# Performance work log

Hardware: AMD Instinct MI355X
Metric: run time of the kernel (lower is better)

The kernel has to match this reference:

```python
import jax, jax.numpy as jnp
import numpy as np

B, S, HID, NH = 64, 197, 768, 12
DH = HID // NH  # 64
EPS = 1e-24


def setup_inputs() -> dict:
    key = jax.random.key(0)
    ks = jax.random.split(key, 20)
    def lin(i):
        w = jax.random.normal(ks[i], (HID, HID), jnp.float32) * 0.02  # stored [in, out]
        b = jnp.zeros((HID,), jnp.float32)
        return w, b
    Wmq, bmq = lin(0); Wcq, bcq = lin(1)
    Wmk, bmk = lin(2); Wck, bck = lin(3)
    Wmv, bmv = lin(4); Wcv, bcv = lin(5)
    Wmd, bmd = lin(6); Wcd, bcd = lin(7)
    return dict(
        input_mean_tensor=jax.random.normal(ks[8], (B, S, HID), jnp.float32),
        input_cov_tensor=jax.random.normal(ks[9], (B, S, HID), jnp.float32),
        Wmq=Wmq, bmq=bmq, Wcq=Wcq, bcq=bcq,
        Wmk=Wmk, bmk=bmk, Wck=Wck, bck=bck,
        Wmv=Wmv, bmv=bmv, Wcv=Wcv, bcv=bcv,
        Wmd=Wmd, bmd=bmd, Wcd=Wcd, bcd=bcd,
    )


def _heads(x):
    # [B, S, HID] -> [B, NH, S, DH]
    return x.reshape(x.shape[0], x.shape[1], NH, DH).transpose(0, 2, 1, 3)


def _merge(x):
    # [B, NH, S, DH] -> [B, S, HID]
    return x.transpose(0, 2, 1, 3).reshape(x.shape[0], x.shape[2], HID)


def wasserstein_distance_matmul(m1, c1, m2, c2):
    # all [B, NH, S, DH]; returns [B, NH, S, S]
    m1_2 = jnp.sum(m1 * m1, -1, keepdims=True)            # [B,NH,S,1]
    m2_2 = jnp.sum(m2 * m2, -1, keepdims=True)
    ret = m1_2 + jnp.swapaxes(m2_2, -1, -2) - 2.0 * jnp.einsum('bhqd,bhkd->bhqk', m1, m2)
    c1_2 = jnp.sum(c1, -1, keepdims=True)
    c2_2 = jnp.sum(c2, -1, keepdims=True)
    s1 = jnp.sqrt(jnp.clip(c1, EPS, None))
    s2 = jnp.sqrt(jnp.clip(c2, EPS, None))
    cov_ret = c1_2 + jnp.swapaxes(c2_2, -1, -2) - 2.0 * jnp.einsum('bhqd,bhkd->bhqk', s1, s2)
    return ret + cov_ret


def reference(input_mean_tensor, input_cov_tensor,
              Wmq, bmq, Wcq, bcq, Wmk, bmk, Wck, bck,
              Wmv, bmv, Wcv, bcv, Wmd, bmd, Wcd, bcd):
    mean_q = _heads(input_mean_tensor @ Wmq + bmq)
    mean_k = _heads(input_mean_tensor @ Wmk + bmk)
    mean_v = _heads(input_mean_tensor @ Wmv + bmv)
    cov_q = _heads(jax.nn.elu(input_cov_tensor @ Wcq + bcq) + 1.0)
    cov_k = _heads(jax.nn.elu(input_cov_tensor @ Wck + bck) + 1.0)
    cov_v = _heads(jax.nn.elu(input_cov_tensor @ Wcv + bcv) + 1.0)

    scores = -wasserstein_distance_matmul(mean_q, cov_q, mean_k, cov_k)
    scores = scores / jnp.sqrt(jnp.float32(DH))
    probs = jax.nn.softmax(scores, axis=-1)  # [B,NH,S,S]

    mean_ctx = _merge(jnp.einsum('bhqk,bhkd->bhqd', probs, mean_v))
    cov_ctx = _merge(jnp.einsum('bhqk,bhkd->bhqd', probs * probs, cov_v))

    mean_hidden = mean_ctx @ Wmd + bmd
    cov_hidden = cov_ctx @ Wcd + bcd
    return (mean_hidden, cov_hidden)
```

## Files before the change

### kernel.cpp

```cpp
#include <hip/hip_runtime.h>
#include <hip/hip_bf16.h>
#include <stdint.h>

typedef _Float16 f16;
typedef _Float16 f16x8 __attribute__((ext_vector_type(8)));
typedef _Float16 f16x4 __attribute__((ext_vector_type(4)));
typedef float f32x4 __attribute__((ext_vector_type(4)));

constexpr int B = 64, S = 197, HID = 768, NH = 12, DH = 64;
constexpr int M = B * S;
constexpr int Mpad = 12800;
constexpr int BNS = B * NH * S;
constexpr int VSTRIDE = 224;
constexpr size_t NPH = (size_t)Mpad * HID;
constexpr size_t MH = (size_t)M * HID;
constexpr size_t WSZ1 = (size_t)HID * HID;
constexpr size_t VTSZ = (size_t)B * NH * DH * VSTRIDE;

__device__ __forceinline__ f32x4 mfma16(f16x8 a, f16x8 b, f32x4 c) {
  return __builtin_amdgcn_mfma_f32_16x16x32_f16(a, b, c, 0, 0, 0);
}

__device__ __forceinline__ void gload16(const void* g, void* l) {
  __builtin_amdgcn_global_load_lds(
      (const __attribute__((address_space(1))) void*)g,
      (__attribute__((address_space(3))) void*)l, 16, 0, 0);
}

__device__ __forceinline__ int xcd_swizzle(int wg, int nwg) {
  const int q = nwg >> 3, r = nwg & 7;
  const int x = wg & 7, p = wg >> 3;
  return (x < r ? x * (q + 1) : r * (q + 1) + (x - r) * q) + p;
}

__global__ __launch_bounds__(256) void zero_kernel(char* __restrict__ p, size_t n16) {
  const size_t i = (size_t)blockIdx.x * 256 + threadIdx.x;
  if (i < n16) reinterpret_cast<int4*>(p)[i] = int4{0, 0, 0, 0};
}

__global__ __launch_bounds__(256) void cvt_x_kernel(
    const float* __restrict__ xm, const float* __restrict__ xc,
    f16* __restrict__ ym, f16* __restrict__ yc) {
  const size_t i8 = ((size_t)blockIdx.x * 256 + threadIdx.x) * 8;
  f16x8 vm = {}, vc = {};
  if (i8 < MH) {
    const float4 a0 = *reinterpret_cast<const float4*>(xm + i8);
    const float4 a1 = *reinterpret_cast<const float4*>(xm + i8 + 4);
    const float4 b0 = *reinterpret_cast<const float4*>(xc + i8);
    const float4 b1 = *reinterpret_cast<const float4*>(xc + i8 + 4);
    vm[0] = (f16)a0.x; vm[1] = (f16)a0.y; vm[2] = (f16)a0.z; vm[3] = (f16)a0.w;
    vm[4] = (f16)a1.x; vm[5] = (f16)a1.y; vm[6] = (f16)a1.z; vm[7] = (f16)a1.w;
    vc[0] = (f16)b0.x; vc[1] = (f16)b0.y; vc[2] = (f16)b0.z; vc[3] = (f16)b0.w;
    vc[4] = (f16)b1.x; vc[5] = (f16)b1.y; vc[6] = (f16)b1.z; vc[7] = (f16)b1.w;
  }
  *reinterpret_cast<f16x8*>(ym + i8) = vm;
  *reinterpret_cast<f16x8*>(yc + i8) = vc;
}

struct WPtrs { const float* w[8]; };

__global__ __launch_bounds__(256) void cvt_w_kernel(WPtrs p, f16* __restrict__ wt) {
  __shared__ float tile[32][33];
  const int z = blockIdx.z;
  const float* W = p.w[z];
  f16* Wt = wt + (size_t)z * WSZ1;
  const int k0 = blockIdx.x * 32, n0 = blockIdx.y * 32;
  const int tx = threadIdx.x & 31, ty = threadIdx.x >> 5;
#pragma unroll
  for (int i = 0; i < 4; ++i)
    tile[ty + i * 8][tx] = W[(size_t)(k0 + ty + i * 8) * HID + n0 + tx];
  __syncthreads();
#pragma unroll
  for (int i = 0; i < 4; ++i)
    Wt[(size_t)(n0 + ty + i * 8) * HID + k0 + tx] = (f16)tile[tx][ty + i * 8];
}

__device__ __forceinline__ void gemm_core(
    const f16* __restrict__ Abase, const f16* __restrict__ Btbase,
    int m0, int n0, int tid, char* lds, f32x4 (&acc)[8][4]) {
  const int w = tid >> 6, lane = tid & 63;
  const int l15 = lane & 15, lg = lane >> 4;
  const int wr = (w >> 2) * 128, wc = (w & 3) * 64;

  const int srow = w * 32 + (lane >> 2);
  const int scol = (lane & 3) * 16;
  const char* gA = reinterpret_cast<const char*>(Abase + (size_t)(m0 + srow) * HID) + scol;
  const char* gB = reinterpret_cast<const char*>(Btbase + (size_t)(n0 + srow) * HID) + scol;
  const int wbase = w * 2048;

#define STAGE_TILE(T, BUF)                                               \
  do {                                                                   \
    const size_t off_ = (size_t)(T) * 64;                                \
    char* la_ = lds + (BUF) * 32768 + wbase;                             \
    char* lb_ = la_ + 16384;                                             \
    gload16(gA + off_, la_);                                             \
    gload16(gA + off_ + (size_t)16 * 1536, la_ + 1024);                  \
    gload16(gB + off_, lb_);                                             \
    gload16(gB + off_ + (size_t)16 * 1536, lb_ + 1024);                  \
  } while (0)

  STAGE_TILE(0, 0);
  STAGE_TILE(1, 1);
  asm volatile("s_waitcnt vmcnt(4)\n\ts_barrier" ::: "memory");

#pragma unroll
  for (int t = 0; t < 24; ++t) {
    if (t + 2 < 24) STAGE_TILE(t + 2, (t + 2) % 3);

    const char* cA = lds + (t % 3) * 32768;
    const char* cB = cA + 16384;
    f16x8 af[8], bf[4];
#pragma unroll
    for (int fi = 0; fi < 8; ++fi)
      af[fi] = *reinterpret_cast<const f16x8*>(cA + (wr + l15 + fi * 16) * 64 + lg * 16);
#pragma unroll
    for (int fj = 0; fj < 4; ++fj)
      bf[fj] = *reinterpret_cast<const f16x8*>(cB + (wc + l15 + fj * 16) * 64 + lg * 16);

    __builtin_amdgcn_s_setprio(1);
#pragma unroll
    for (int fi = 0; fi < 8; ++fi)
#pragma unroll
      for (int fj = 0; fj < 4; ++fj)
        acc[fi][fj] = mfma16(af[fi], bf[fj], acc[fi][fj]);
    __builtin_amdgcn_s_setprio(0);

    if (t + 2 < 24) {
      asm volatile("s_waitcnt vmcnt(4)\n\ts_barrier" ::: "memory");
    } else if (t + 1 < 24) {
      asm volatile("s_waitcnt vmcnt(0)\n\ts_barrier" ::: "memory");
    }
  }
#undef STAGE_TILE
}

struct ProjArgs {
  const f16* A[2]; const f16* Bt[2];
  const float* bias[2][3];
  f16* out0[2];
  f16* out1[2];
  f16* vt[2];
  float* qterm; float* kterm;
};

__global__ __launch_bounds__(512, 1) void gemm_proj(ProjArgs g) {
  __shared__ alignas(16) char lds[98304];
  const int swz = xcd_swizzle(blockIdx.x, 900);
  const int z = swz / 450;
  const int rest = swz - z * 450;
  const int x = rest / 9, y = rest - x * 9;
  const int m0 = x * 256, n0 = y * 256;

  f32x4 acc[8][4] = {};
  gemm_core(g.A[z], g.Bt[z], m0, n0, threadIdx.x, lds, acc);

  const int tid = threadIdx.x, w = tid >> 6, lane = tid & 63;
  const int l15 = lane & 15, lg = lane >> 4;
  const int wr = (w >> 2) * 128, wc = (w & 3) * 64;
  const int nsel = n0 / 768;
  const int colbase = (n0 - nsel * 768) + wc;
  const int rbase = m0 + wr + lg * 4;
  const float* bias = g.bias[z][nsel];
  const int hh = colbase >> 6;

  if (nsel < 2) {
    f16* Y = nsel ? g.out1[z] : g.out0[z];
    float* term = nsel ? g.kterm : g.qterm;
    float bv4[4];
#pragma unroll
    for (int fj = 0; fj < 4; ++fj) bv4[fj] = bias[colbase + l15 + fj * 16];
#pragma unroll
    for (int fi = 0; fi < 8; ++fi) {
#pragma unroll
      for (int r = 0; r < 4; ++r) {
        const int row = rbase + fi * 16 + r;
        float ssum = 0.f;
#pragma unroll
        for (int fj = 0; fj < 4; ++fj) {
          float v = acc[fi][fj][r] + bv4[fj];
          if (z == 1) { v = (v > 0.f) ? v + 1.f : __expf(v); v = sqrtf(v); }
          const f16 st = (f16)(v * 0.5f);
          if (row < M) Y[(size_t)row * HID + colbase + l15 + fj * 16] = st;
          const float sf = (float)st;
          ssum = fmaf(sf, sf, ssum);
        }
        ssum += __shfl_xor(ssum, 1, 64);
        ssum += __shfl_xor(ssum, 2, 64);
        ssum += __shfl_xor(ssum, 4, 64);
        ssum += __shfl_xor(ssum, 8, 64);
        if (l15 == 0 && row < M) {
          const int bb = row / S, ss = row - bb * S;
          atomicAdd(&term[(bb * NH + hh) * S + ss], 0.5f * ssum);
        }
      }
    }
  } else {
    f16* VT = g.vt[z];
#pragma unroll
    for (int fj = 0; fj < 4; ++fj) {
      const int col = colbase + l15 + fj * 16;
      const float bv = bias[col];
      const int dd = col & 63;
#pragma unroll
      for (int fi = 0; fi < 8; ++fi)
#pragma unroll
        for (int r = 0; r < 4; ++r) {
          const int row = rbase + fi * 16 + r;
          if (row < M) {
            float v = acc[fi][fj][r] + bv;
            if (z == 1) v = (v > 0.f) ? v + 1.f : __expf(v);
            const int bb = row / S, ss = row - bb * S;
            VT[((size_t)(bb * NH + hh) * DH + dd) * VSTRIDE + ss] = (f16)v;
          }
        }
    }
  }
}

struct OutArgs {
  const f16* A[2]; const f16* Bt[2]; const float* bias[2]; float* Y[2];
};

__global__ __launch_bounds__(512, 1) void gemm_out(OutArgs g) {
  __shared__ alignas(16) char lds[98304];
  const int swz = xcd_swizzle(blockIdx.x, 300);
  const int z = swz / 150;
  const int rest = swz - z * 150;
  const int x = rest / 3, y = rest - x * 3;
  const int m0 = x * 256, n0 = y * 256;

  f32x4 acc[8][4] = {};
  gemm_core(g.A[z], g.Bt[z], m0, n0, threadIdx.x, lds, acc);

  const int tid = threadIdx.x, w = tid >> 6, lane = tid & 63;
  const int l15 = lane & 15, lg = lane >> 4;
  const int wr = (w >> 2) * 128, wc = (w & 3) * 64;
  const int rbase = m0 + wr + lg * 4;
  float* Y = g.Y[z];
#pragma unroll
  for (int fj = 0; fj < 4; ++fj) {
    const int col = n0 + wc + l15 + fj * 16;
    const float bv = g.bias[z][col];
#pragma unroll
    for (int fi = 0; fi < 8; ++fi)
#pragma unroll
      for (int r = 0; r < 4; ++r) {
        const int row = rbase + fi * 16 + r;
        if (row < M) Y[(size_t)row * HID + col] = acc[fi][fj][r] + bv;
      }
  }
}

__global__ __launch_bounds__(256, 2) void attn_kernel(
    const f16* __restrict__ mq, const f16* __restrict__ sq,
    const f16* __restrict__ mk, const f16* __restrict__ sk,
    const f16* __restrict__ vtm, const f16* __restrict__ vtc,
    const float* __restrict__ qterm, const float* __restrict__ kterm,
    f16* __restrict__ mean_ctx, f16* __restrict__ cov_ctx) {
  __shared__ char Pb[64 * 512];
  __shared__ float qt_s[64];
  __shared__ float kt_s[256];
  __shared__ float red_m[4][64];
  __shared__ float red_s[4][64];

  const int swz = xcd_swizzle(blockIdx.x, 3072);
  const int qtile = swz & 3, bh = swz >> 2;
  const int h = bh % NH, b = bh / NH;
  const int s0 = qtile * 64;
  const int tid = threadIdx.x, w = tid >> 6, lane = tid & 63;
  const int l15 = lane & 15, lg = lane >> 4;

  const size_t base = (size_t)(b * S) * HID + (size_t)h * DH;
  const int tb = bh * S;

  f16x8 qmf[4][2], qsf[4][2];
#pragma unroll
  for (int fi = 0; fi < 4; ++fi) {
    const size_t o = base + (size_t)(s0 + fi * 16 + l15) * HID + lg * 8;
    qmf[fi][0] = *reinterpret_cast<const f16x8*>(mq + o);
    qmf[fi][1] = *reinterpret_cast<const f16x8*>(mq + o + 32);
    qsf[fi][0] = *reinterpret_cast<const f16x8*>(sq + o);
    qsf[fi][1] = *reinterpret_cast<const f16x8*>(sq + o + 32);
  }
  if (tid < 64) qt_s[tid] = (s0 + tid < S) ? qterm[tb + s0 + tid] : 0.f;
  kt_s[tid] = (tid < S) ? kterm[tb + tid] : 0.f;
  __syncthreads();

  f32x4 acc[4][4] = {};
  __builtin_amdgcn_s_setprio(1);
#pragma unroll
  for (int fj = 0; fj < 4; ++fj) {
    const size_t o = base + (size_t)(w * 64 + fj * 16 + l15) * HID + lg * 8;
    const f16x8 a0 = *reinterpret_cast<const f16x8*>(mk + o);
    const f16x8 a1 = *reinterpret_cast<const f16x8*>(mk + o + 32);
    const f16x8 c0 = *reinterpret_cast<const f16x8*>(sk + o);
    const f16x8 c1 = *reinterpret_cast<const f16x8*>(sk + o + 32);
#pragma unroll
    for (int fi = 0; fi < 4; ++fi) {
      acc[fj][fi] = mfma16(a0, qmf[fi][0], acc[fj][fi]);
      acc[fj][fi] = mfma16(c0, qsf[fi][0], acc[fj][fi]);
      acc[fj][fi] = mfma16(a1, qmf[fi][1], acc[fj][fi]);
      acc[fj][fi] = mfma16(c1, qsf[fi][1], acc[fj][fi]);
    }
  }
  __builtin_amdgcn_s_setprio(0);

  const int d = w * 16 + l15;
  const size_t vbase = ((size_t)bh * DH + d) * VSTRIDE + lg * 8;
  f16x8 vmr[7], vcr[7];
#pragma unroll
  for (int ks = 0; ks < 7; ++ks) {
    vmr[ks] = *reinterpret_cast<const f16x8*>(vtm + vbase + ks * 32);
    vcr[ks] = *reinterpret_cast<const f16x8*>(vtc + vbase + ks * 32);
  }

#pragma unroll
  for (int fi = 0; fi < 4; ++fi) {
    const float qv = qt_s[fi * 16 + l15];
    float mx = -1e30f;
#pragma unroll
    for (int fj = 0; fj < 4; ++fj)
#pragma unroll
      for (int r = 0; r < 4; ++r) {
        const int j = w * 64 + fj * 16 + lg * 4 + r;
        float sv = acc[fj][fi][r] - qv - kt_s[j];
        if (j >= S) sv = -1e30f;
        acc[fj][fi][r] = sv;
        mx = fmaxf(mx, sv);
      }
    mx = fmaxf(mx, __shfl_xor(mx, 16, 64));
    mx = fmaxf(mx, __shfl_xor(mx, 32, 64));
    if (lg == 0) red_m[w][fi * 16 + l15] = mx;
  }
  __syncthreads();

#pragma unroll
  for (int fi = 0; fi < 4; ++fi) {
    const int q = fi * 16 + l15;
    const float m = fmaxf(fmaxf(red_m[0][q], red_m[1][q]),
                          fmaxf(red_m[2][q], red_m[3][q]));
    const int xr = (q & 7) << 4;
    float sum = 0.f;
#pragma unroll
    for (int fj = 0; fj < 4; ++fj) {
      f16x4 p4;
#pragma unroll
      for (int r = 0; r < 4; ++r) {
        const float e = __expf(acc[fj][fi][r] - m);
        sum += e;
        p4[r] = (f16)e;
      }
      *reinterpret_cast<f16x4*>(
          Pb + q * 512 + ((2 * (w * 64 + fj * 16 + lg * 4)) ^ xr)) = p4;
    }
    sum += __shfl_xor(sum, 16, 64);
    sum += __shfl_xor(sum, 32, 64);
    if (lg == 0) red_s[w][q] = sum;
  }
  __syncthreads();

  f32x4 macc[4] = {}, cacc[4] = {};
  __builtin_amdgcn_s_setprio(1);
#pragma unroll
  for (int ks = 0; ks < 7; ++ks) {
#pragma unroll
    for (int fi = 0; fi < 4; ++fi) {
      const int q = fi * 16 + l15;
      const f16x8 pa = *reinterpret_cast<const f16x8*>(
          Pb + q * 512 + ((2 * (ks * 32 + lg * 8)) ^ ((q & 7) << 4)));
      macc[fi] = mfma16(pa, vmr[ks], macc[fi]);
      const f16x8 pq = pa * pa;
      cacc[fi] = mfma16(pq, vcr[ks], cacc[fi]);
    }
  }
  __builtin_amdgcn_s_setprio(0);

#pragma unroll
  for (int fi = 0; fi < 4; ++fi)
#pragma unroll
    for (int r = 0; r < 4; ++r) {
      const int qo = fi * 16 + lg * 4 + r;
      const int srow = s0 + qo;
      if (srow < S) {
        const float tot = red_s[0][qo] + red_s[1][qo] + red_s[2][qo] + red_s[3][qo];
        const float inv = 1.f / tot;
        const size_t oidx = (size_t)(b * S + srow) * HID + h * DH + d;
        mean_ctx[oidx] = (f16)(macc[fi][r] * inv);
        cov_ctx[oidx] = (f16)(cacc[fi][r] * inv * inv);
      }
    }
}

extern "C" void kernel_launch(void* const* d_in, const int* in_sizes, int n_in,
                              void* d_out, int out_size, void* d_ws, size_t ws_size,
                              hipStream_t stream) {
  const float* in_mean = (const float*)d_in[0];
  const float* in_cov = (const float*)d_in[1];
  const float* Wmq = (const float*)d_in[2];  const float* bmq = (const float*)d_in[3];
  const float* Wcq = (const float*)d_in[4];  const float* bcq = (const float*)d_in[5];
  const float* Wmk = (const float*)d_in[6];  const float* bmk = (const float*)d_in[7];
  const float* Wck = (const float*)d_in[8];  const float* bck = (const float*)d_in[9];
  const float* Wmv = (const float*)d_in[10]; const float* bmv = (const float*)d_in[11];
  const float* Wcv = (const float*)d_in[12]; const float* bcv = (const float*)d_in[13];
  const float* Wmd = (const float*)d_in[14]; const float* bmd = (const float*)d_in[15];
  const float* Wcd = (const float*)d_in[16]; const float* bcd = (const float*)d_in[17];

  const size_t need = (2 * NPH + 8 * WSZ1 + 4 * MH + 2 * VTSZ) * sizeof(f16) +
                      2 * (size_t)BNS * sizeof(float);
  if (ws_size < need) return;

  f16* Xm = (f16*)d_ws;
  f16* Xc = Xm + NPH;
  f16* Wt = Xc + NPH;
  f16* mq = Wt + 8 * WSZ1;
  f16* mk = mq + MH;
  f16* sq = mk + MH;
  f16* sk = sq + MH;
  f16* vtm = sk + MH;
  f16* vtc = vtm + VTSZ;
  float* qterm = (float*)(vtc + VTSZ);
  float* kterm = qterm + BNS;
  f16* mean_ctx = Xm;
  f16* cov_ctx = Xc;

  float* out_mean = (float*)d_out;
  float* out_cov = out_mean + MH;

  dim3 blk(256);

  const size_t zbytes = 2 * VTSZ * sizeof(f16) + 2 * (size_t)BNS * sizeof(float);
  const size_t n16 = zbytes / 16;
  zero_kernel<<<(int)((n16 + 255) / 256), blk, 0, stream>>>((char*)vtm, n16);

  cvt_x_kernel<<<(int)(NPH / 2048), blk, 0, stream>>>(in_mean, in_cov, Xm, Xc);

  WPtrs wp;
  wp.w[0] = Wmq; wp.w[1] = Wmk; wp.w[2] = Wmv;
  wp.w[3] = Wcq; wp.w[4] = Wck; wp.w[5] = Wcv;
  wp.w[6] = Wmd; wp.w[7] = Wcd;
  cvt_w_kernel<<<dim3(24, 24, 8), blk, 0, stream>>>(wp, Wt);

  ProjArgs pa;
  pa.A[0] = Xm; pa.A[1] = Xc;
  pa.Bt[0] = Wt; pa.Bt[1] = Wt + 3 * WSZ1;
  pa.bias[0][0] = bmq; pa.bias[0][1] = bmk; pa.bias[0][2] = bmv;
  pa.bias[1][0] = bcq; pa.bias[1][1] = bck; pa.bias[1][2] = bcv;
  pa.out0[0] = mq; pa.out0[1] = sq;
  pa.out1[0] = mk; pa.out1[1] = sk;
  pa.vt[0] = vtm; pa.vt[1] = vtc;
  pa.qterm = qterm; pa.kterm = kterm;
  gemm_proj<<<900, dim3(512), 0, stream>>>(pa);

  attn_kernel<<<3072, blk, 0, stream>>>(mq, sq, mk, sk, vtm, vtc,
                                        qterm, kterm, mean_ctx, cov_ctx);

  OutArgs oa;
  oa.A[0] = mean_ctx; oa.A[1] = cov_ctx;
  oa.Bt[0] = Wt + 6 * WSZ1; oa.Bt[1] = Wt + 7 * WSZ1;
  oa.bias[0] = bmd; oa.bias[1] = bcd;
  oa.Y[0] = out_mean; oa.Y[1] = out_cov;
  gemm_out<<<300, dim3(512), 0, stream>>>(oa);
}
```

Before: 376.4 us.

## Restructure GEMM core to 64-wide K tiles with XOR-swizzled LDS and interleaved staging

```diff
diff --git a/kernel.cpp b/kernel.cpp
--- a/kernel.cpp
+++ b/kernel.cpp
@@ -82,56 +82,108 @@
   const int l15 = lane & 15, lg = lane >> 4;
   const int wr = (w >> 2) * 128, wc = (w & 3) * 64;
 
-  const int srow = w * 32 + (lane >> 2);
-  const int scol = (lane & 3) * 16;
-  const char* gA = reinterpret_cast<const char*>(Abase + (size_t)(m0 + srow) * HID) + scol;
-  const char* gB = reinterpret_cast<const char*>(Btbase + (size_t)(n0 + srow) * HID) + scol;
-  const int wbase = w * 2048;
-
-#define STAGE_TILE(T, BUF)                                               \
-  do {                                                                   \
-    const size_t off_ = (size_t)(T) * 64;                                \
-    char* la_ = lds + (BUF) * 32768 + wbase;                             \
-    char* lb_ = la_ + 16384;                                             \
-    gload16(gA + off_, la_);                                             \
-    gload16(gA + off_ + (size_t)16 * 1536, la_ + 1024);                  \
-    gload16(gB + off_, lb_);                                             \
-    gload16(gB + off_ + (size_t)16 * 1536, lb_ + 1024);                  \
+  const int lrow = w * 8 + (lane >> 3);
+  const int lslot = ((lane & 7) ^ ((lane >> 3) & 7)) * 16;
+  const char* gA = reinterpret_cast<const char*>(Abase + (size_t)(m0 + lrow) * HID) + lslot;
+  const char* gB = reinterpret_cast<const char*>(Btbase + (size_t)(n0 + lrow) * HID) + lslot;
+  const int wrow = w * 8;
+
+  const int sK0 = (((0 + lg) ^ (l15 & 7)) * 16);
+  const int sK1 = (((4 + lg) ^ (l15 & 7)) * 16);
+
+  f16x8 af[8][2], bf[4][2];
+
+#define STG_A(k, d, h, g)                                                   \
+  gload16(gA + (size_t)((h) * 128 + (g) * 64) * 1536 + (k) * 128,           \
+          lds + (d) * 65536 + ((h) * 128 + (g) * 64 + wrow) * 128)
+#define STG_B(k, d, h, g)                                                   \
+  gload16(gB + (size_t)((h) * 128 + (g) * 64) * 1536 + (k) * 128,           \
+          lds + (d) * 65536 + 32768 + ((h) * 128 + (g) * 64 + wrow) * 128)
+#define STG_AH(k, d, h) do { STG_A(k, d, h, 0); STG_A(k, d, h, 1); } while (0)
+#define STG_BH(k, d, h) do { STG_B(k, d, h, 0); STG_B(k, d, h, 1); } while (0)
+
+#define READS_P0(d)                                                          \
+  do {                                                                       \
+    const char* base_ = lds + (d) * 65536;                                   \
+    _Pragma("unroll") for (int fi = 0; fi < 4; ++fi) {                       \
+      af[fi][0] = *reinterpret_cast<const f16x8*>(                           \
+          base_ + (wr + l15 + fi * 16) * 128 + sK0);                         \
+      af[fi][1] = *reinterpret_cast<const f16x8*>(                           \
+          base_ + (wr + l15 + fi * 16) * 128 + sK1);                         \
+    }                                                                        \
+    _Pragma("unroll") for (int fj = 0; fj < 4; ++fj)                         \
+      bf[fj][0] = *reinterpret_cast<const f16x8*>(                           \
+          base_ + 32768 + (wc + l15 + fj * 16) * 128 + sK0);                 \
   } while (0)
-
-  STAGE_TILE(0, 0);
-  STAGE_TILE(1, 1);
-  asm volatile("s_waitcnt vmcnt(4)\n\ts_barrier" ::: "memory");
-
-#pragma unroll
-  for (int t = 0; t < 24; ++t) {
-    if (t + 2 < 24) STAGE_TILE(t + 2, (t + 2) % 3);
-
-    const char* cA = lds + (t % 3) * 32768;
-    const char* cB = cA + 16384;
-    f16x8 af[8], bf[4];
-#pragma unroll
-    for (int fi = 0; fi < 8; ++fi)
-      af[fi] = *reinterpret_cast<const f16x8*>(cA + (wr + l15 + fi * 16) * 64 + lg * 16);
-#pragma unroll
-    for (int fj = 0; fj < 4; ++fj)
-      bf[fj] = *reinterpret_cast<const f16x8*>(cB + (wc + l15 + fj * 16) * 64 + lg * 16);
-
-    __builtin_amdgcn_s_setprio(1);
-#pragma unroll
-    for (int fi = 0; fi < 8; ++fi)
-#pragma unroll
-      for (int fj = 0; fj < 4; ++fj)
-        acc[fi][fj] = mfma16(af[fi], bf[fj], acc[fi][fj]);
-    __builtin_amdgcn_s_setprio(0);
-
-    if (t + 2 < 24) {
-      asm volatile("s_waitcnt vmcnt(4)\n\ts_barrier" ::: "memory");
-    } else if (t + 1 < 24) {
-      asm volatile("s_waitcnt vmcnt(0)\n\ts_barrier" ::: "memory");
-    }
-  }
-#undef STAGE_TILE
+#define READS_P1(d)                                                          \
+  do {                                                                       \
+    const char* base_ = lds + (d) * 65536;                                   \
+    _Pragma("unroll") for (int fi = 4; fi < 8; ++fi) {                       \
+      af[fi][0] = *reinterpret_cast<const f16x8*>(                           \
+          base_ + (wr + l15 + fi * 16) * 128 + sK0);                         \
+      af[fi][1] = *reinterpret_cast<const f16x8*>(                           \
+          base_ + (wr + l15 + fi * 16) * 128 + sK1);                         \
+    }                                                                        \
+    _Pragma("unroll") for (int fj = 0; fj < 4; ++fj)                         \
+      bf[fj][1] = *reinterpret_cast<const f16x8*>(                           \
+          base_ + 32768 + (wc + l15 + fj * 16) * 128 + sK1);                 \
+  } while (0)
+
+#define MFMA_Q(fib, ks)                                                      \
+  do {                                                                       \
+    __builtin_amdgcn_s_setprio(1);                                           \
+    _Pragma("unroll") for (int fi = (fib); fi < (fib) + 4; ++fi)             \
+      _Pragma("unroll") for (int fj = 0; fj < 4; ++fj)                       \
+        acc[fi][fj] = mfma16(af[fi][ks], bf[fj][ks], acc[fi][fj]);           \
+    __builtin_amdgcn_s_setprio(0);                                           \
+  } while (0)
+
+#define BAR asm volatile("s_barrier" ::: "memory")
+#define LGK0 asm volatile("s_waitcnt lgkmcnt(0)" ::: "memory")
+#define VMC4_BAR asm volatile("s_waitcnt vmcnt(4)\n\ts_barrier" ::: "memory")
+#define VMC0_BAR asm volatile("s_waitcnt vmcnt(0)\n\ts_barrier" ::: "memory")
+
+  STG_AH(0, 0, 0); STG_AH(0, 0, 1); STG_BH(0, 0, 0); STG_BH(0, 0, 1);
+  STG_AH(1, 1, 0); STG_AH(1, 1, 1); STG_BH(1, 1, 0); STG_BH(1, 1, 1);
+  asm volatile("s_waitcnt vmcnt(8)\n\ts_barrier" ::: "memory");
+
+#pragma unroll
+  for (int i = 0; i < 6; ++i) {
+    const int k1 = 2 * i + 1, kn0 = 2 * i + 2, kn1 = 2 * i + 3;
+    READS_P0(0);
+    if (i > 0) STG_BH(k1, 1, 0);
+    BAR; LGK0; MFMA_Q(0, 0); BAR;
+    READS_P1(0);
+    if (i > 0) STG_BH(k1, 1, 1);
+    BAR; LGK0; MFMA_Q(4, 0); BAR;
+    if (i < 5) STG_AH(kn0, 0, 0);
+    BAR; LGK0; MFMA_Q(0, 1); BAR;
+    if (i < 5) STG_AH(kn0, 0, 1);
+    BAR; LGK0; MFMA_Q(4, 1);
+    if (i < 5) { VMC4_BAR; } else { VMC0_BAR; }
+    READS_P0(1);
+    if (i < 5) STG_BH(kn0, 0, 0);
+    BAR; LGK0; MFMA_Q(0, 0); BAR;
+    READS_P1(1);
+    if (i < 5) STG_BH(kn0, 0, 1);
+    BAR; LGK0; MFMA_Q(4, 0); BAR;
+    if (i < 5) STG_AH(kn1, 1, 0);
+    BAR; LGK0; MFMA_Q(0, 1); BAR;
+    if (i < 5) STG_AH(kn1, 1, 1);
+    BAR; LGK0; MFMA_Q(4, 1);
+    if (i < 5) { VMC4_BAR; }
+  }
+#undef STG_A
+#undef STG_B
+#undef STG_AH
+#undef STG_BH
+#undef READS_P0
+#undef READS_P1
+#undef MFMA_Q
+#undef BAR
+#undef LGK0
+#undef VMC4_BAR
+#undef VMC0_BAR
 }
 
 struct ProjArgs {
@@ -143,8 +195,8 @@
   float* qterm; float* kterm;
 };
 
-__global__ __launch_bounds__(512, 1) void gemm_proj(ProjArgs g) {
-  __shared__ alignas(16) char lds[98304];
+__global__ __launch_bounds__(512, 2) void gemm_proj(ProjArgs g) {
+  __shared__ alignas(16) char lds[131072];
   const int swz = xcd_swizzle(blockIdx.x, 900);
   const int z = swz / 450;
   const int rest = swz - z * 450;
@@ -221,8 +273,8 @@
   const f16* A[2]; const f16* Bt[2]; const float* bias[2]; float* Y[2];
 };
 
-__global__ __launch_bounds__(512, 1) void gemm_out(OutArgs g) {
-  __shared__ alignas(16) char lds[98304];
+__global__ __launch_bounds__(512, 2) void gemm_out(OutArgs g) {
+  __shared__ alignas(16) char lds[131072];
   const int swz = xcd_swizzle(blockIdx.x, 300);
   const int z = swz / 150;
   const int rest = swz - z * 150;
```

Result: no change. 369.2 us (-1.9%).
